# Kernel tuning notes

Measured on AMD Instinct MI355X. Metric: run time of the kernel, lower is better.

## Reference

```python
import jax, jax.numpy as jnp
import numpy as np

TEMP = 8.0      # config.router_temp
TOP_K = 2       # config.moe_top_k
EPS = 1e-8
LN_EPS = 1e-5


def _layer_norm_noaffine(x):
    # nn.LayerNorm(input_dim, elementwise_affine=False)
    mu = jnp.mean(x, axis=-1, keepdims=True)
    var = jnp.var(x, axis=-1, keepdims=True)
    return (x - mu) / jnp.sqrt(var + LN_EPS)


def _unit_norm(x):
    # x / x.norm(dim=-1).clamp(min=EPS)
    n = jnp.linalg.norm(x, axis=-1, keepdims=True)
    return x / jnp.maximum(n, EPS)


def setup_inputs() -> dict:
    key = jax.random.key(0)
    k1, k2 = jax.random.split(key)
    x = jax.random.normal(k1, (4, 4096, 2048), dtype=jnp.float32)
    prototypes = jax.random.normal(k2, (64, 2048), dtype=jnp.float32)
    return {"x": x, "prototypes": prototypes}


def reference(x, prototypes):
    # input_norm_fn = 'norm_d', proto_norm_fn = 'unit'
    xn = _layer_norm_noaffine(x)          # [b, s, d]
    pn = _unit_norm(prototypes)           # [e, d]
    logits = jnp.einsum('bsd,ed->bse', xn, pn) / TEMP   # [b, s, e]
    probs = jax.nn.softmax(logits, axis=-1)
    top_w, top_i = jax.lax.top_k(probs, TOP_K)          # [b, s, k]
    top_w = top_w / jnp.sum(top_w, axis=-1, keepdims=True)
    return top_w, top_i
```

## Files before the change

kernel.cpp:

```cpp
#include <hip/hip_runtime.h>
#include <math.h>

typedef __attribute__((ext_vector_type(8))) short short8;
typedef __attribute__((ext_vector_type(4))) float f32x4;

constexpr int kD  = 2048;
constexpr int kE  = 64;
constexpr int kM  = 16;
constexpr int kBK = 128;
constexpr int kIt = kD / kBK;
constexpr int kCS = 3136;

constexpr int kPlaneU = 4 * 64 * 512;
__device__ unsigned short g_B[3 * kPlaneU];

__device__ __forceinline__ void split3(float v, unsigned& h, unsigned& m, unsigned& l) {
  unsigned u = __float_as_uint(v);
  h = u & 0xFFFF0000u;
  float r1 = v - __uint_as_float(h);
  m = __float_as_uint(r1) & 0xFFFF0000u;
  float r2 = r1 - __uint_as_float(m);
  l = __float_as_uint(r2);
}

__device__ __forceinline__ void pack2(float e0, float e1,
                                      unsigned& dh, unsigned& dm, unsigned& dl) {
  unsigned h0, m0, l0, h1, m1, l1;
  split3(e0, h0, m0, l0);
  split3(e1, h1, m1, l1);
  dh = (h0 >> 16) | h1;
  dm = (m0 >> 16) | m1;
  dl = (l0 >> 16) | (l1 & 0xFFFF0000u);
}

__global__ __launch_bounds__(256) void proto_prep(const float* __restrict__ p,
                                                  float* __restrict__ ws) {
  const int e = blockIdx.x, t = threadIdx.x;
  const float* row = p + (size_t)e * kD;
  float4 v0 = *(const float4*)(row + 8 * t);
  float4 v1 = *(const float4*)(row + 8 * t + 4);

  unsigned dh[4], dm[4], dl[4];
  pack2(v0.x, v0.y, dh[0], dm[0], dl[0]);
  pack2(v0.z, v0.w, dh[1], dm[1], dl[1]);
  pack2(v1.x, v1.y, dh[2], dm[2], dl[2]);
  pack2(v1.z, v1.w, dh[3], dm[3], dl[3]);
  const int gc = t >> 2, o = t & 3;
  size_t base = (size_t)((e >> 4) * 64 + gc) * 512 + (16 * o + (e & 15)) * 8;
  *(uint4*)&g_B[base]               = make_uint4(dh[0], dh[1], dh[2], dh[3]);
  *(uint4*)&g_B[kPlaneU + base]     = make_uint4(dm[0], dm[1], dm[2], dm[3]);
  *(uint4*)&g_B[2 * kPlaneU + base] = make_uint4(dl[0], dl[1], dl[2], dl[3]);

  float s = (v0.x + v0.y) + (v0.z + v0.w) + (v1.x + v1.y) + (v1.z + v1.w);
  float q = v0.x*v0.x + v0.y*v0.y + v0.z*v0.z + v0.w*v0.w
          + v1.x*v1.x + v1.y*v1.y + v1.z*v1.z + v1.w*v1.w;
  #pragma unroll
  for (int off = 32; off >= 1; off >>= 1) {
    s += __shfl_xor(s, off, 64);
    q += __shfl_xor(q, off, 64);
  }
  __shared__ float as[4], aq[4];
  if ((t & 63) == 0) { as[t >> 6] = s; aq[t >> 6] = q; }
  __syncthreads();
  if (t == 0) {
    float S = (as[0] + as[1]) + (as[2] + as[3]);
    float Q = (aq[0] + aq[1]) + (aq[2] + aq[3]);
    ws[e]      = S;
    ws[kE + e] = 1.f / fmaxf(sqrtf(Q), 1e-8f);
  }
}

__global__ __launch_bounds__(256, 4) void router_main(
    const float* __restrict__ x, const float* __restrict__ ws,
    float* __restrict__ out_w, float* __restrict__ out_i) {
  __shared__ __align__(16) unsigned char sA[4 * kCS];
  __shared__ float sLogit[kM * 68];
  __shared__ float sStats[kM][2];

  const int t    = threadIdx.x;
  const int w    = t >> 6;
  const int L    = t & 63;
  const int ln15 = L & 15;
  const int q    = L >> 4;
  const int tok0 = blockIdx.x * kM;
  const float* xg = x + (size_t)tok0 * kD;

  f32x4 acc = (f32x4){0.f, 0.f, 0.f, 0.f};
  float sx[2] = {0.f, 0.f}, sxx[2] = {0.f, 0.f};

  float4 pf[2];
  #pragma unroll
  for (int jj = 0; jj < 2; ++jj) {
    int f = t + 256 * jj;
    pf[jj] = *(const float4*)(xg + (size_t)(f >> 5) * kD + (f & 31) * 4);
  }

  for (int it = 0; it < kIt; ++it) {
    __syncthreads();
    #pragma unroll
    for (int jj = 0; jj < 2; ++jj) {
      int f = t + 256 * jj;
      int c4 = f & 31, k = 4 * c4;
      int m = f >> 5, c = k >> 5, o = (k >> 3) & 3, j = k & 7;
      float4 v = pf[jj];
      sx[jj] += (v.x + v.y) + (v.z + v.w);
      sxx[jj] = fmaf(v.x, v.x, fmaf(v.y, v.y, fmaf(v.z, v.z, fmaf(v.w, v.w, sxx[jj]))));
      unsigned dh0, dm0, dl0, dh1, dm1, dl1;
      pack2(v.x, v.y, dh0, dm0, dl0);
      pack2(v.z, v.w, dh1, dm1, dl1);
      unsigned char* dst = sA + c * kCS + (16 * o + m) * 48 + o * 16 + j * 2;
      *(uint2*)(dst)      = make_uint2(dh0, dh1);
      *(uint2*)(dst + 16) = make_uint2(dm0, dm1);
      *(uint2*)(dst + 32) = make_uint2(dl0, dl1);
    }
    __syncthreads();
    if (it + 1 < kIt) {
      #pragma unroll
      for (int jj = 0; jj < 2; ++jj) {
        int f = t + 256 * jj;
        pf[jj] = *(const float4*)(xg + (size_t)(f >> 5) * kD + (it + 1) * kBK + (f & 31) * 4);
      }
    }
    #pragma unroll
    for (int c = 0; c < 4; ++c) {
      const int gc = it * 4 + c;
      const size_t bo = (size_t)(w * 64 + gc) * 512 + L * 8;
      short8 bh = *(const short8*)&g_B[bo];
      short8 bm = *(const short8*)&g_B[kPlaneU + bo];
      short8 bl = *(const short8*)&g_B[2 * kPlaneU + bo];
      const unsigned char* ra = sA + c * kCS + L * 48 + (L >> 4) * 16;
      short8 ah = *(const short8*)(ra);
      short8 am = *(const short8*)(ra + 16);
      short8 al = *(const short8*)(ra + 32);
      acc = __builtin_amdgcn_mfma_f32_16x16x32_bf16(ah, bh, acc, 0, 0, 0);
      acc = __builtin_amdgcn_mfma_f32_16x16x32_bf16(ah, bm, acc, 0, 0, 0);
      acc = __builtin_amdgcn_mfma_f32_16x16x32_bf16(am, bh, acc, 0, 0, 0);
      acc = __builtin_amdgcn_mfma_f32_16x16x32_bf16(am, bm, acc, 0, 0, 0);
      acc = __builtin_amdgcn_mfma_f32_16x16x32_bf16(ah, bl, acc, 0, 0, 0);
      acc = __builtin_amdgcn_mfma_f32_16x16x32_bf16(al, bh, acc, 0, 0, 0);
    }
  }

  #pragma unroll
  for (int jj = 0; jj < 2; ++jj) {
    float a = sx[jj], b = sxx[jj];
    #pragma unroll
    for (int off = 16; off >= 1; off >>= 1) {
      a += __shfl_xor(a, off, 64);
      b += __shfl_xor(b, off, 64);
    }
    if ((L & 31) == 0) {
      int m = (t >> 5) + 8 * jj;
      sStats[m][0] = a;
      sStats[m][1] = b;
    }
  }

  #pragma unroll
  for (int i = 0; i < 4; ++i)
    sLogit[(q * 4 + i) * 68 + w * 16 + ln15] = acc[i];
  __syncthreads();

  const float Se  = ws[L];
  const float inv = ws[kE + L];
  #pragma unroll
  for (int tl = 0; tl < 4; ++tl) {
    int tk = w * 4 + tl;
    float mu   = sStats[tk][0] * (1.f / kD);
    float var  = sStats[tk][1] * (1.f / kD) - mu * mu;
    float rstd = rsqrtf(var + 1e-5f);
    float logit = (sLogit[tk * 68 + L] - mu * Se) * rstd * inv * 0.125f;

    float v1 = logit; int i1 = L;
    #pragma unroll
    for (int off = 32; off >= 1; off >>= 1) {
      float ov = __shfl_xor(v1, off, 64);
      int   oi = __shfl_xor(i1, off, 64);
      if (ov > v1 || (ov == v1 && oi < i1)) { v1 = ov; i1 = oi; }
    }
    float ml = (L == i1) ? -3.402823466e38f : logit;
    float v2 = ml; int i2 = L;
    #pragma unroll
    for (int off = 32; off >= 1; off >>= 1) {
      float ov = __shfl_xor(v2, off, 64);
      int   oi = __shfl_xor(i2, off, 64);
      if (ov > v2 || (ov == v2 && oi < i2)) { v2 = ov; i2 = oi; }
    }
    if (L == 0) {
      int tg = tok0 + tk;
      float er = expf(v2 - v1);
      float r  = 1.f / (1.f + er);
      out_w[2 * tg]     = r;
      out_w[2 * tg + 1] = er * r;
      out_i[2 * tg]     = (float)i1;
      out_i[2 * tg + 1] = (float)i2;
    }
  }
}

extern "C" void kernel_launch(void* const* d_in, const int* in_sizes, int n_in,
                              void* d_out, int out_size, void* d_ws, size_t ws_size,
                              hipStream_t stream) {
  const float* x = (const float*)d_in[0];
  const float* p = (const float*)d_in[1];
  float* ws = (float*)d_ws;
  const int T = in_sizes[0] / kD;
  float* out_w = (float*)d_out;
  float* out_i = (float*)d_out + (size_t)T * 2;

  proto_prep<<<kE, 256, 0, stream>>>(p, ws);
  router_main<<<T / kM, 256, 0, stream>>>(x, ws, out_w, out_i);
}
```

Measured before the change: 225.2 us.

## Load x fragments directly into registers per wave, dropping LDS staging

Removes the shared-memory staging of split bf16 x tiles and the two barriers per K-step. Each wave now loads its own x fragment from global memory, splits it into hi/mid/lo bf16 in registers and feeds the MFMAs, with a two-deep register prefetch. The prototype buffer is re-laid out so the three planes for each chunk sit next to each other. The trade-off is that all four waves re-read the same x rows and redo the split conversion, relying on cache hits instead of LDS sharing.

Result: slower. 261.5 us (+16.1%).

```diff
diff --git a/kernel.cpp b/kernel.cpp
--- a/kernel.cpp
+++ b/kernel.cpp
@@ -7,12 +7,9 @@
 constexpr int kD  = 2048;
 constexpr int kE  = 64;
 constexpr int kM  = 16;
-constexpr int kBK = 128;
-constexpr int kIt = kD / kBK;
-constexpr int kCS = 3136;
+constexpr int kGC = kD / 32;
 
-constexpr int kPlaneU = 4 * 64 * 512;
-__device__ unsigned short g_B[3 * kPlaneU];
+__device__ unsigned short g_B[4 * 64 * 3 * 512];
 
 __device__ __forceinline__ void split3(float v, unsigned& h, unsigned& m, unsigned& l) {
   unsigned u = __float_as_uint(v);
@@ -33,6 +30,8 @@
   dl = (l0 >> 16) | (l1 & 0xFFFF0000u);
 }
 
+union FragU { short8 s; unsigned u[4]; };
+
 __global__ __launch_bounds__(256) void proto_prep(const float* __restrict__ p,
                                                   float* __restrict__ ws) {
   const int e = blockIdx.x, t = threadIdx.x;
@@ -46,10 +45,11 @@
   pack2(v1.x, v1.y, dh[2], dm[2], dl[2]);
   pack2(v1.z, v1.w, dh[3], dm[3], dl[3]);
   const int gc = t >> 2, o = t & 3;
-  size_t base = (size_t)((e >> 4) * 64 + gc) * 512 + (16 * o + (e & 15)) * 8;
-  *(uint4*)&g_B[base]               = make_uint4(dh[0], dh[1], dh[2], dh[3]);
-  *(uint4*)&g_B[kPlaneU + base]     = make_uint4(dm[0], dm[1], dm[2], dm[3]);
-  *(uint4*)&g_B[2 * kPlaneU + base] = make_uint4(dl[0], dl[1], dl[2], dl[3]);
+  const int Lr = 16 * o + (e & 15);
+  size_t cb = (size_t)(((e >> 4) * 64 + gc) * 3) * 512 + Lr * 8;
+  *(uint4*)&g_B[cb]          = make_uint4(dh[0], dh[1], dh[2], dh[3]);
+  *(uint4*)&g_B[cb + 512]    = make_uint4(dm[0], dm[1], dm[2], dm[3]);
+  *(uint4*)&g_B[cb + 1024]   = make_uint4(dl[0], dl[1], dl[2], dl[3]);
 
   float s = (v0.x + v0.y) + (v0.z + v0.w) + (v1.x + v1.y) + (v1.z + v1.w);
   float q = v0.x*v0.x + v0.y*v0.y + v0.z*v0.z + v0.w*v0.w
@@ -73,7 +73,6 @@
 __global__ __launch_bounds__(256, 4) void router_main(
     const float* __restrict__ x, const float* __restrict__ ws,
     float* __restrict__ out_w, float* __restrict__ out_i) {
-  __shared__ __align__(16) unsigned char sA[4 * kCS];
   __shared__ float sLogit[kM * 68];
   __shared__ float sStats[kM][2];
 
@@ -83,77 +82,58 @@
   const int ln15 = L & 15;
   const int q    = L >> 4;
   const int tok0 = blockIdx.x * kM;
-  const float* xg = x + (size_t)tok0 * kD;
+
+  const float* xa = x + (size_t)(tok0 + ln15) * kD + q * 8;
+  const unsigned short* bp = g_B + (size_t)w * (64 * 3 * 512) + L * 8;
 
   f32x4 acc = (f32x4){0.f, 0.f, 0.f, 0.f};
-  float sx[2] = {0.f, 0.f}, sxx[2] = {0.f, 0.f};
+  float sx = 0.f, sxx = 0.f;
 
-  float4 pf[2];
-  #pragma unroll
-  for (int jj = 0; jj < 2; ++jj) {
-    int f = t + 256 * jj;
-    pf[jj] = *(const float4*)(xg + (size_t)(f >> 5) * kD + (f & 31) * 4);
+  float4 xv[2][2];
+  short8 bv[3];
+  xv[0][0] = *(const float4*)(xa);
+  xv[0][1] = *(const float4*)(xa + 4);
+  xv[1][0] = *(const float4*)(xa + 32);
+  xv[1][1] = *(const float4*)(xa + 36);
+  bv[0] = *(const short8*)(bp);
+  bv[1] = *(const short8*)(bp + 512);
+  bv[2] = *(const short8*)(bp + 1024);
+
+  #pragma unroll 4
+  for (int gc = 0; gc < kGC; ++gc) {
+    float4 v0 = xv[gc & 1][0], v1 = xv[gc & 1][1];
+    short8 bh = bv[0], bm = bv[1], bl = bv[2];
+    if (gc + 1 < kGC) {
+      const unsigned short* nb = bp + (size_t)(gc + 1) * 1536;
+      bv[0] = *(const short8*)(nb);
+      bv[1] = *(const short8*)(nb + 512);
+      bv[2] = *(const short8*)(nb + 1024);
+    }
+    if (gc + 2 < kGC) {
+      xv[gc & 1][0] = *(const float4*)(xa + (gc + 2) * 32);
+      xv[gc & 1][1] = *(const float4*)(xa + (gc + 2) * 32 + 4);
+    }
+    sx += (v0.x + v0.y) + (v0.z + v0.w) + (v1.x + v1.y) + (v1.z + v1.w);
+    sxx = fmaf(v0.x, v0.x, fmaf(v0.y, v0.y, fmaf(v0.z, v0.z, fmaf(v0.w, v0.w, sxx))));
+    sxx = fmaf(v1.x, v1.x, fmaf(v1.y, v1.y, fmaf(v1.z, v1.z, fmaf(v1.w, v1.w, sxx))));
+    FragU ah, am, al;
+    pack2(v0.x, v0.y, ah.u[0], am.u[0], al.u[0]);
+    pack2(v0.z, v0.w, ah.u[1], am.u[1], al.u[1]);
+    pack2(v1.x, v1.y, ah.u[2], am.u[2], al.u[2]);
+    pack2(v1.z, v1.w, ah.u[3], am.u[3], al.u[3]);
+    acc = __builtin_amdgcn_mfma_f32_16x16x32_bf16(ah.s, bh, acc, 0, 0, 0);
+    acc = __builtin_amdgcn_mfma_f32_16x16x32_bf16(ah.s, bm, acc, 0, 0, 0);
+    acc = __builtin_amdgcn_mfma_f32_16x16x32_bf16(am.s, bh, acc, 0, 0, 0);
+    acc = __builtin_amdgcn_mfma_f32_16x16x32_bf16(am.s, bm, acc, 0, 0, 0);
+    acc = __builtin_amdgcn_mfma_f32_16x16x32_bf16(ah.s, bl, acc, 0, 0, 0);
+    acc = __builtin_amdgcn_mfma_f32_16x16x32_bf16(al.s, bh, acc, 0, 0, 0);
   }
 
-  for (int it = 0; it < kIt; ++it) {
-    __syncthreads();
-    #pragma unroll
-    for (int jj = 0; jj < 2; ++jj) {
-      int f = t + 256 * jj;
-      int c4 = f & 31, k = 4 * c4;
-      int m = f >> 5, c = k >> 5, o = (k >> 3) & 3, j = k & 7;
-      float4 v = pf[jj];
-      sx[jj] += (v.x + v.y) + (v.z + v.w);
-      sxx[jj] = fmaf(v.x, v.x, fmaf(v.y, v.y, fmaf(v.z, v.z, fmaf(v.w, v.w, sxx[jj]))));
-      unsigned dh0, dm0, dl0, dh1, dm1, dl1;
-      pack2(v.x, v.y, dh0, dm0, dl0);
-      pack2(v.z, v.w, dh1, dm1, dl1);
-      unsigned char* dst = sA + c * kCS + (16 * o + m) * 48 + o * 16 + j * 2;
-      *(uint2*)(dst)      = make_uint2(dh0, dh1);
-      *(uint2*)(dst + 16) = make_uint2(dm0, dm1);
-      *(uint2*)(dst + 32) = make_uint2(dl0, dl1);
-    }
-    __syncthreads();
-    if (it + 1 < kIt) {
-      #pragma unroll
-      for (int jj = 0; jj < 2; ++jj) {
-        int f = t + 256 * jj;
-        pf[jj] = *(const float4*)(xg + (size_t)(f >> 5) * kD + (it + 1) * kBK + (f & 31) * 4);
-      }
-    }
-    #pragma unroll
-    for (int c = 0; c < 4; ++c) {
-      const int gc = it * 4 + c;
-      const size_t bo = (size_t)(w * 64 + gc) * 512 + L * 8;
-      short8 bh = *(const short8*)&g_B[bo];
-      short8 bm = *(const short8*)&g_B[kPlaneU + bo];
-      short8 bl = *(const short8*)&g_B[2 * kPlaneU + bo];
-      const unsigned char* ra = sA + c * kCS + L * 48 + (L >> 4) * 16;
-      short8 ah = *(const short8*)(ra);
-      short8 am = *(const short8*)(ra + 16);
-      short8 al = *(const short8*)(ra + 32);
-      acc = __builtin_amdgcn_mfma_f32_16x16x32_bf16(ah, bh, acc, 0, 0, 0);
-      acc = __builtin_amdgcn_mfma_f32_16x16x32_bf16(ah, bm, acc, 0, 0, 0);
-      acc = __builtin_amdgcn_mfma_f32_16x16x32_bf16(am, bh, acc, 0, 0, 0);
-      acc = __builtin_amdgcn_mfma_f32_16x16x32_bf16(am, bm, acc, 0, 0, 0);
-      acc = __builtin_amdgcn_mfma_f32_16x16x32_bf16(ah, bl, acc, 0, 0, 0);
-      acc = __builtin_amdgcn_mfma_f32_16x16x32_bf16(al, bh, acc, 0, 0, 0);
-    }
-  }
-
-  #pragma unroll
-  for (int jj = 0; jj < 2; ++jj) {
-    float a = sx[jj], b = sxx[jj];
-    #pragma unroll
-    for (int off = 16; off >= 1; off >>= 1) {
-      a += __shfl_xor(a, off, 64);
-      b += __shfl_xor(b, off, 64);
-    }
-    if ((L & 31) == 0) {
-      int m = (t >> 5) + 8 * jj;
-      sStats[m][0] = a;
-      sStats[m][1] = b;
-    }
+  sx  += __shfl_xor(sx, 16, 64);  sx  += __shfl_xor(sx, 32, 64);
+  sxx += __shfl_xor(sxx, 16, 64); sxx += __shfl_xor(sxx, 32, 64);
+  if (w == 0 && q == 0) {
+    sStats[ln15][0] = sx;
+    sStats[ln15][1] = sxx;
   }
 
   #pragma unroll
```
